# Kernel tuning notes

Measured on AMD Instinct MI355X. Metric: run time of the kernel, lower is better.

Reference implementation:

```python
import jax, jax.numpy as jnp
import numpy as np

THRESHOLD = 0.3
STRENGTH = 0.1
MIN_S = 0.0
MAX_S = 0.5
EPS_COS = 1e-8
EPS_LN = 1e-5

B, T, D = 1024, 64, 256
P = 2048
H = 512


def _layernorm(x, g, b):
    mu = x.mean(-1, keepdims=True)
    var = ((x - mu) ** 2).mean(-1, keepdims=True)
    return (x - mu) * jax.lax.rsqrt(var + EPS_LN) * g + b


def setup_inputs() -> dict:
    key = jax.random.key(0)
    ks = jax.random.split(key, 10)
    s = lambda fan_in: 1.0 / np.sqrt(fan_in)
    return {
        "current_feat": jax.random.normal(ks[0], (B, T, D), jnp.float32),
        "prototype": jax.random.normal(ks[1], (P, T, D), jnp.float32),
        "dd_w1": jax.random.normal(ks[2], (2 * D, H), jnp.float32) * s(2 * D),
        "dd_b1": jnp.zeros((H,), jnp.float32),
        "dd_g1": jnp.ones((H,), jnp.float32),
        "dd_be1": jnp.zeros((H,), jnp.float32),
        "dd_w2": jax.random.normal(ks[3], (H, H // 2), jnp.float32) * s(H),
        "dd_b2": jnp.zeros((H // 2,), jnp.float32),
        "dd_w3": jax.random.normal(ks[4], (H // 2, 1), jnp.float32) * s(H // 2),
        "dd_b3": jnp.zeros((1,), jnp.float32),
        "cal_w1": jax.random.normal(ks[5], (D, H), jnp.float32) * s(D),
        "cal_b1": jnp.zeros((H,), jnp.float32),
        "cal_g1": jnp.ones((H,), jnp.float32),
        "cal_be1": jnp.zeros((H,), jnp.float32),
        "cal_w2": jax.random.normal(ks[6], (H, H), jnp.float32) * s(H),
        "cal_b2": jnp.zeros((H,), jnp.float32),
        "cal_w3": jax.random.normal(ks[7], (H, D), jnp.float32) * s(H),
        "cal_b3": jnp.zeros((D,), jnp.float32),
    }


def reference(current_feat, prototype,
              dd_w1, dd_b1, dd_g1, dd_be1, dd_w2, dd_b2, dd_w3, dd_b3,
              cal_w1, cal_b1, cal_g1, cal_be1, cal_w2, cal_b2, cal_w3, cal_b3):
    # --- drift detection ---
    feat_flat = current_feat.mean(axis=1)          # [B, D]
    proto_centers = prototype.mean(axis=1)         # [P, D]
    fn = jnp.maximum(jnp.linalg.norm(feat_flat, axis=-1), EPS_COS)   # [B]
    pn = jnp.maximum(jnp.linalg.norm(proto_centers, axis=-1), EPS_COS)  # [P]
    sim = jnp.einsum('bd,pd->bp', feat_flat, proto_centers) / (fn[:, None] * pn[None, :])
    drift_score = 1.0 - sim                        # [B, P]
    is_drifted = drift_score.mean(axis=0) > THRESHOLD  # [P] bool

    # --- calibration (batched over all P, then masked scatter) ---
    global_mean = feat_flat.mean(axis=0)           # [D]
    concat = jnp.concatenate(
        [proto_centers, jnp.broadcast_to(global_mean, (proto_centers.shape[0], global_mean.shape[0]))], axis=-1)  # [P, 2D]
    h = jax.nn.relu(_layernorm(concat @ dd_w1 + dd_b1, dd_g1, dd_be1))
    h = jax.nn.relu(h @ dd_w2 + dd_b2)
    drift_conf = jax.nn.sigmoid(h @ dd_w3 + dd_b3)[:, 0]  # [P]

    c = jax.nn.relu(_layernorm(proto_centers @ cal_w1 + cal_b1, cal_g1, cal_be1))
    c = jax.nn.relu(c @ cal_w2 + cal_b2)
    delta = c @ cal_w3 + cal_b3                    # [P, D]

    strength = jnp.clip(STRENGTH * drift_conf, MIN_S, MAX_S)  # [P]
    new_center = proto_centers + strength[:, None] * delta    # [P, D]

    calibrated = jnp.where(is_drifted[:, None, None], new_center[:, None, :], prototype)  # [P, T, D]
    return calibrated, drift_score, is_drifted
```

## Files before the change

kernel.cpp:

```cpp
#include <hip/hip_runtime.h>
#include <hip/hip_bf16.h>
#include <math.h>

#define BB 1024
#define TT 64
#define DD 256
#define PP 2048
#define HH 512

typedef __attribute__((ext_vector_type(8))) short short8;
typedef __attribute__((ext_vector_type(4))) short short4v;
typedef __attribute__((ext_vector_type(4))) float f32x4;

__device__ __forceinline__ float4 f4add(float4 a, float4 b) {
    return make_float4(a.x + b.x, a.y + b.y, a.z + b.z, a.w + b.w);
}

__device__ __forceinline__ void nt_store4(float* p, float4 v) {
    f32x4 t = {v.x, v.y, v.z, v.w};
    __builtin_nontemporal_store(t, (f32x4*)p);
}

__device__ __forceinline__ void nt_store1(float* p, float v) {
    __builtin_nontemporal_store(v, p);
}

__device__ __forceinline__ float4 nt_load4(const float* p) {
    f32x4 t = __builtin_nontemporal_load((const f32x4*)p);
    return make_float4(t.x, t.y, t.z, t.w);
}

__device__ __forceinline__ void store_bf16x4(__hip_bfloat16* dst, float4 m) {
    union { __hip_bfloat16 h[4]; short4v s; } u;
    u.h[0] = __float2bfloat16(m.x); u.h[1] = __float2bfloat16(m.y);
    u.h[2] = __float2bfloat16(m.z); u.h[3] = __float2bfloat16(m.w);
    *(short4v*)dst = u.s;
}

__global__ void prep_k(const float* __restrict__ cf, const float* __restrict__ proto,
                       const float* __restrict__ dd_w1, const float* __restrict__ dd_w2,
                       const float* __restrict__ cal_w1, const float* __restrict__ cal_w2,
                       const float* __restrict__ cal_w3,
                       float* __restrict__ ffm, float* __restrict__ fn,
                       float* __restrict__ pn, float* __restrict__ pc,
                       float* __restrict__ colsum,
                       __hip_bfloat16* __restrict__ ffb, __hip_bfloat16* __restrict__ pcb,
                       __hip_bfloat16* __restrict__ w1cat, __hip_bfloat16* __restrict__ w2dd,
                       __hip_bfloat16* __restrict__ w2cal, __hip_bfloat16* __restrict__ w3cal) {
    int b = blockIdx.x, tid = threadIdx.x;
    if (b < 768) {
        int wv = tid >> 6, lane = tid & 63;
        int row = (b << 2) + wv;
        const float* base = (row < 1024) ? cf + (size_t)row * TT * DD
                                         : proto + (size_t)(row - 1024) * TT * DD;
        const float* p = base + (lane << 2);
        float4 acc = make_float4(0.f, 0.f, 0.f, 0.f);
        float4 v[16];
        #pragma unroll
        for (int tb = 0; tb < TT; tb += 16) {
            #pragma unroll
            for (int i = 0; i < 16; ++i)
                v[i] = nt_load4(p + (size_t)(tb + i) * DD);
            #pragma unroll
            for (int i = 0; i < 8; ++i) v[i] = f4add(v[i], v[i + 8]);
            #pragma unroll
            for (int i = 0; i < 4; ++i) v[i] = f4add(v[i], v[i + 4]);
            acc = f4add(acc, f4add(f4add(v[0], v[1]), f4add(v[2], v[3])));
        }
        float4 m = make_float4(acc.x * (1.f / TT), acc.y * (1.f / TT),
                               acc.z * (1.f / TT), acc.w * (1.f / TT));
        if (row < 1024) {
            *(float4*)(ffm + (size_t)row * DD + (lane << 2)) = m;
            store_bf16x4(ffb + (size_t)row * DD + (lane << 2), m);
        } else {
            int r = row - 1024;
            *(float4*)(pc + (size_t)r * DD + (lane << 2)) = m;
            store_bf16x4(pcb + (size_t)r * DD + (lane << 2), m);
        }
        float q = m.x * m.x + m.y * m.y + m.z * m.z + m.w * m.w;
        #pragma unroll
        for (int o = 32; o > 0; o >>= 1) q += __shfl_xor(q, o, 64);
        if (lane == 0) {
            float nv = fmaxf(sqrtf(q), 1e-8f);
            if (row < 1024) fn[row] = nv; else pn[row - 1024] = nv;
        }
    } else {
        int bb = b - 768;
        if (bb < 8) colsum[bb * 256 + tid] = 0.f;
        #pragma unroll
        for (int i2 = 0; i2 < 4; ++i2) {
            int idx = bb * 1024 + i2 * 256 + tid;
            if (idx < 262144) {
                int half = idx >> 17;
                int i = idx & 131071;
                int n = i & 511, k = i >> 9;
                const float* src = half ? cal_w1 : dd_w1;
                float x = __builtin_nontemporal_load(src + (size_t)k * 512 + n);
                w1cat[(size_t)(half * 512 + n) * 256 + k] = __float2bfloat16(x);
            } else if (idx < 393216) {
                int i = idx - 262144;
                int n = i & 255, k = i >> 8;
                float x = __builtin_nontemporal_load(dd_w2 + (size_t)k * 256 + n);
                w2dd[(size_t)n * 512 + k] = __float2bfloat16(x);
            } else if (idx < 655360) {
                int i = idx - 393216;
                int n = i & 511, k = i >> 9;
                float x = __builtin_nontemporal_load(cal_w2 + (size_t)k * 512 + n);
                w2cal[(size_t)n * 512 + k] = __float2bfloat16(x);
            } else {
                int i = idx - 655360;
                int n = i & 255, k = i >> 8;
                float x = __builtin_nontemporal_load(cal_w3 + (size_t)k * 256 + n);
                w3cal[(size_t)n * 512 + k] = __float2bfloat16(x);
            }
        }
    }
}

__global__ void sim_addvec_k(const __hip_bfloat16* __restrict__ A,
                             const __hip_bfloat16* __restrict__ Bt,
                             const float* __restrict__ fn, const float* __restrict__ pn,
                             const float* __restrict__ ffm,
                             const float* __restrict__ dd_w1, const float* __restrict__ dd_b1,
                             float* __restrict__ drift, float* __restrict__ colsum,
                             float* __restrict__ addvec) {
    if (blockIdx.x >= 512) {
        __shared__ float gmk[256];
        int tid = threadIdx.x;
        const float* f = ffm + tid;
        float a0 = 0.f, a1 = 0.f, a2 = 0.f, a3 = 0.f, a4 = 0.f, a5 = 0.f, a6 = 0.f, a7 = 0.f;
        #pragma unroll 4
        for (int b = 0; b < 1024; b += 8) {
            a0 += f[(b + 0) << 8]; a1 += f[(b + 1) << 8];
            a2 += f[(b + 2) << 8]; a3 += f[(b + 3) << 8];
            a4 += f[(b + 4) << 8]; a5 += f[(b + 5) << 8];
            a6 += f[(b + 6) << 8]; a7 += f[(b + 7) << 8];
        }
        gmk[tid] = (((a0 + a1) + (a2 + a3)) + ((a4 + a5) + (a6 + a7))) * (1.f / BB);
        __syncthreads();
        int j = (blockIdx.x - 512) * 256 + tid;
        float s = dd_b1[j];
        #pragma unroll 8
        for (int k = 0; k < 256; ++k) s = fmaf(gmk[k], dd_w1[(size_t)(256 + k) * 512 + j], s);
        addvec[j] = s;
        return;
    }
    int wid = (blockIdx.x << 2) + (threadIdx.x >> 6);
    int lane = threadIdx.x & 63;
    int mw = wid >> 6, nw = wid & 63;
    int m0 = mw << 5, n0 = nw << 5;
    int lr = lane & 15, quad = lane >> 4;
    const __hip_bfloat16* pa0 = A + (size_t)(m0 + lr) * DD + quad * 8;
    const __hip_bfloat16* pa1 = pa0 + 16 * DD;
    const __hip_bfloat16* pb0 = Bt + (size_t)(n0 + lr) * DD + quad * 8;
    const __hip_bfloat16* pb1 = pb0 + 16 * DD;
    f32x4 acc00 = {0,0,0,0}, acc01 = {0,0,0,0}, acc10 = {0,0,0,0}, acc11 = {0,0,0,0};
    #pragma unroll
    for (int k = 0; k < DD; k += 32) {
        short8 a0 = *(const short8*)(pa0 + k);
        short8 a1 = *(const short8*)(pa1 + k);
        short8 b0 = *(const short8*)(pb0 + k);
        short8 b1 = *(const short8*)(pb1 + k);
        acc00 = __builtin_amdgcn_mfma_f32_16x16x32_bf16(a0, b0, acc00, 0, 0, 0);
        acc01 = __builtin_amdgcn_mfma_f32_16x16x32_bf16(a0, b1, acc01, 0, 0, 0);
        acc10 = __builtin_amdgcn_mfma_f32_16x16x32_bf16(a1, b0, acc10, 0, 0, 0);
        acc11 = __builtin_amdgcn_mfma_f32_16x16x32_bf16(a1, b1, acc11, 0, 0, 0);
    }
    int col0 = n0 + lr, col1 = col0 + 16;
    float ip0 = 1.f / pn[col0], ip1 = 1.f / pn[col1];
    float cs0 = 0.f, cs1 = 0.f;
    #pragma unroll
    for (int r = 0; r < 4; ++r) {
        int row0 = m0 + quad * 4 + r;
        int row1 = row0 + 16;
        float if0 = 1.f / fn[row0];
        float if1 = 1.f / fn[row1];
        float d00 = 1.f - acc00[r] * if0 * ip0;
        float d01 = 1.f - acc01[r] * if0 * ip1;
        float d10 = 1.f - acc10[r] * if1 * ip0;
        float d11 = 1.f - acc11[r] * if1 * ip1;
        nt_store1(&drift[(size_t)row0 * PP + col0], d00);
        nt_store1(&drift[(size_t)row0 * PP + col1], d01);
        nt_store1(&drift[(size_t)row1 * PP + col0], d10);
        nt_store1(&drift[(size_t)row1 * PP + col1], d11);
        cs0 += d00 + d10;
        cs1 += d01 + d11;
    }
    cs0 += __shfl_xor(cs0, 16, 64); cs0 += __shfl_xor(cs0, 32, 64);
    cs1 += __shfl_xor(cs1, 16, 64); cs1 += __shfl_xor(cs1, 32, 64);
    if (quad == 0) {
        atomicAdd(&colsum[col0], cs0);
        atomicAdd(&colsum[col1], cs1);
    }
}

__global__ void gemm1ln_k(const __hip_bfloat16* __restrict__ pcb,
                          const __hip_bfloat16* __restrict__ w1cat,
                          const float* __restrict__ addvec, const float* __restrict__ cal_b1,
                          const float* __restrict__ gdd, const float* __restrict__ bedd,
                          const float* __restrict__ gcal, const float* __restrict__ becal,
                          __hip_bfloat16* __restrict__ Ydd, __hip_bfloat16* __restrict__ Ycal) {
    __shared__ float lds_s[4][32];
    __shared__ float lds_q[4][32];
    int h = blockIdx.x >> 6;
    int r0 = (blockIdx.x & 63) << 5;
    int wv = threadIdx.x >> 6;
    int lane = threadIdx.x & 63;
    int lr = lane & 15, quad = lane >> 4;
    const float* bias = h ? cal_b1 : addvec;
    const float* g    = h ? gcal : gdd;
    const float* be   = h ? becal : bedd;
    __hip_bfloat16* Y = h ? Ycal : Ydd;

    const __hip_bfloat16* pa0 = pcb + (size_t)(r0 + lr) * DD + quad * 8;
    const __hip_bfloat16* pa1 = pa0 + 16 * DD;

    f32x4 a00[4], a01[4], a10[4], a11[4];
    float bi0[4], bi1[4];
    #pragma unroll
    for (int t = 0; t < 4; ++t) {
        int n0g = h * 512 + wv * 128 + t * 32;
        const __hip_bfloat16* pb0 = w1cat + (size_t)(n0g + lr) * DD + quad * 8;
        const __hip_bfloat16* pb1 = pb0 + 16 * DD;
        f32x4 c00 = {0,0,0,0}, c01 = {0,0,0,0}, c10 = {0,0,0,0}, c11 = {0,0,0,0};
        #pragma unroll
        for (int k = 0; k < DD; k += 32) {
            short8 av0 = *(const short8*)(pa0 + k);
            short8 av1 = *(const short8*)(pa1 + k);
            short8 bv0 = *(const short8*)(pb0 + k);
            short8 bv1 = *(const short8*)(pb1 + k);
            c00 = __builtin_amdgcn_mfma_f32_16x16x32_bf16(av0, bv0, c00, 0, 0, 0);
            c01 = __builtin_amdgcn_mfma_f32_16x16x32_bf16(av0, bv1, c01, 0, 0, 0);
            c10 = __builtin_amdgcn_mfma_f32_16x16x32_bf16(av1, bv0, c10, 0, 0, 0);
            c11 = __builtin_amdgcn_mfma_f32_16x16x32_bf16(av1, bv1, c11, 0, 0, 0);
        }
        a00[t] = c00; a01[t] = c01; a10[t] = c10; a11[t] = c11;
        int cl0 = wv * 128 + t * 32 + lr;
        bi0[t] = bias[cl0];
        bi1[t] = bias[cl0 + 16];
    }

    float ps_lo[4] = {0,0,0,0}, pq_lo[4] = {0,0,0,0};
    float ps_hi[4] = {0,0,0,0}, pq_hi[4] = {0,0,0,0};
    #pragma unroll
    for (int t = 0; t < 4; ++t) {
        #pragma unroll
        for (int r = 0; r < 4; ++r) {
            float v00 = a00[t][r] + bi0[t];
            float v01 = a01[t][r] + bi1[t];
            float v10 = a10[t][r] + bi0[t];
            float v11 = a11[t][r] + bi1[t];
            a00[t][r] = v00; a01[t][r] = v01; a10[t][r] = v10; a11[t][r] = v11;
            ps_lo[r] += v00 + v01;  pq_lo[r] += v00 * v00 + v01 * v01;
            ps_hi[r] += v10 + v11;  pq_hi[r] += v10 * v10 + v11 * v11;
        }
    }
    #pragma unroll
    for (int mset = 1; mset < 16; mset <<= 1) {
        #pragma unroll
        for (int r = 0; r < 4; ++r) {
            ps_lo[r] += __shfl_xor(ps_lo[r], mset, 64);
            pq_lo[r] += __shfl_xor(pq_lo[r], mset, 64);
            ps_hi[r] += __shfl_xor(ps_hi[r], mset, 64);
            pq_hi[r] += __shfl_xor(pq_hi[r], mset, 64);
        }
    }
    if (lr < 8) {
        int rr = quad * 4 + (lr & 3) + ((lr >> 2) << 4);
        lds_s[wv][rr] = (lr >= 4) ? ps_hi[lr & 3] : ps_lo[lr & 3];
        lds_q[wv][rr] = (lr >= 4) ? pq_hi[lr & 3] : pq_lo[lr & 3];
    }
    __syncthreads();

    float mu_lo[4], rs_lo[4], mu_hi[4], rs_hi[4];
    #pragma unroll
    for (int r = 0; r < 4; ++r) {
        int rl = quad * 4 + r;
        float s = lds_s[0][rl] + lds_s[1][rl] + lds_s[2][rl] + lds_s[3][rl];
        float q = lds_q[0][rl] + lds_q[1][rl] + lds_q[2][rl] + lds_q[3][rl];
        float mu = s * (1.f / HH);
        float var = fmaxf(q * (1.f / HH) - mu * mu, 0.f);
        mu_lo[r] = mu; rs_lo[r] = rsqrtf(var + 1e-5f);
        int rh = rl + 16;
        s = lds_s[0][rh] + lds_s[1][rh] + lds_s[2][rh] + lds_s[3][rh];
        q = lds_q[0][rh] + lds_q[1][rh] + lds_q[2][rh] + lds_q[3][rh];
        mu = s * (1.f / HH);
        var = fmaxf(q * (1.f / HH) - mu * mu, 0.f);
        mu_hi[r] = mu; rs_hi[r] = rsqrtf(var + 1e-5f);
    }

    #pragma unroll
    for (int t = 0; t < 4; ++t) {
        int c0 = wv * 128 + t * 32 + lr, c1 = c0 + 16;
        float g0 = g[c0], g1 = g[c1], b0 = be[c0], b1 = be[c1];
        #pragma unroll
        for (int r = 0; r < 4; ++r) {
            int row = r0 + quad * 4 + r;
            float y00 = fmaxf((a00[t][r] - mu_lo[r]) * rs_lo[r] * g0 + b0, 0.f);
            float y01 = fmaxf((a01[t][r] - mu_lo[r]) * rs_lo[r] * g1 + b1, 0.f);
            float y10 = fmaxf((a10[t][r] - mu_hi[r]) * rs_hi[r] * g0 + b0, 0.f);
            float y11 = fmaxf((a11[t][r] - mu_hi[r]) * rs_hi[r] * g1 + b1, 0.f);
            Y[(size_t)row * HH + c0]        = __float2bfloat16(y00);
            Y[(size_t)row * HH + c1]        = __float2bfloat16(y01);
            Y[(size_t)(row + 16) * HH + c0] = __float2bfloat16(y10);
            Y[(size_t)(row + 16) * HH + c1] = __float2bfloat16(y11);
        }
    }
}

template <int K, int OUT_BF16, int RELU>
__device__ __forceinline__ void gemm_tile(const __hip_bfloat16* __restrict__ A,
                                          const __hip_bfloat16* __restrict__ Bt,
                                          const float* __restrict__ bias0,
                                          const float* __restrict__ bias1, int split,
                                          void* __restrict__ Cout, int N, int lognt,
                                          int wid, int lane) {
    int mw = wid >> lognt, nw = wid & ((1 << lognt) - 1);
    int m0 = mw << 5, n0 = nw << 5;
    int lr = lane & 15, quad = lane >> 4;
    const __hip_bfloat16* pa0 = A + (size_t)(m0 + lr) * K + quad * 8;
    const __hip_bfloat16* pa1 = pa0 + 16 * K;
    const __hip_bfloat16* pb0 = Bt + (size_t)(n0 + lr) * K + quad * 8;
    const __hip_bfloat16* pb1 = pb0 + 16 * K;
    f32x4 acc00 = {0,0,0,0}, acc01 = {0,0,0,0}, acc10 = {0,0,0,0}, acc11 = {0,0,0,0};
    #pragma unroll
    for (int k = 0; k < K; k += 32) {
        short8 a0 = *(const short8*)(pa0 + k);
        short8 a1 = *(const short8*)(pa1 + k);
        short8 b0 = *(const short8*)(pb0 + k);
        short8 b1 = *(const short8*)(pb1 + k);
        acc00 = __builtin_amdgcn_mfma_f32_16x16x32_bf16(a0, b0, acc00, 0, 0, 0);
        acc01 = __builtin_amdgcn_mfma_f32_16x16x32_bf16(a0, b1, acc01, 0, 0, 0);
        acc10 = __builtin_amdgcn_mfma_f32_16x16x32_bf16(a1, b0, acc10, 0, 0, 0);
        acc11 = __builtin_amdgcn_mfma_f32_16x16x32_bf16(a1, b1, acc11, 0, 0, 0);
    }
    int col0 = n0 + lr, col1 = col0 + 16;
    float bi0 = (col0 < split) ? bias0[col0] : bias1[col0 - split];
    float bi1 = (col1 < split) ? bias0[col1] : bias1[col1 - split];
    #pragma unroll
    for (int r = 0; r < 4; ++r) {
        int row0 = m0 + quad * 4 + r;
        int row1 = row0 + 16;
        float v00 = acc00[r] + bi0, v01 = acc01[r] + bi1;
        float v10 = acc10[r] + bi0, v11 = acc11[r] + bi1;
        if (RELU) {
            v00 = fmaxf(v00, 0.f); v01 = fmaxf(v01, 0.f);
            v10 = fmaxf(v10, 0.f); v11 = fmaxf(v11, 0.f);
        }
        if (OUT_BF16) {
            __hip_bfloat16* C = (__hip_bfloat16*)Cout;
            C[(size_t)row0 * N + col0] = __float2bfloat16(v00);
            C[(size_t)row0 * N + col1] = __float2bfloat16(v01);
            C[(size_t)row1 * N + col0] = __float2bfloat16(v10);
            C[(size_t)row1 * N + col1] = __float2bfloat16(v11);
        } else {
            float* C = (float*)Cout;
            C[(size_t)row0 * N + col0] = v00;
            C[(size_t)row0 * N + col1] = v01;
            C[(size_t)row1 * N + col0] = v10;
            C[(size_t)row1 * N + col1] = v11;
        }
    }
}

__global__ void gemm2_k(const __hip_bfloat16* __restrict__ act_dd,
                        const __hip_bfloat16* __restrict__ act_cal,
                        const __hip_bfloat16* __restrict__ w2dd,
                        const __hip_bfloat16* __restrict__ w2cal,
                        const float* __restrict__ dd_b2, const float* __restrict__ cal_b2,
                        __hip_bfloat16* __restrict__ act2b, __hip_bfloat16* __restrict__ act3b) {
    int lane = threadIdx.x & 63;
    if (blockIdx.x < 128) {
        int wid = (blockIdx.x << 2) + (threadIdx.x >> 6);
        gemm_tile<512, 1, 1>(act_dd, w2dd, dd_b2, dd_b2, 1 << 30, act2b, 256, 3, wid, lane);
    } else {
        int wid = ((blockIdx.x - 128) << 2) + (threadIdx.x >> 6);
        gemm_tile<512, 1, 1>(act_cal, w2cal, cal_b2, cal_b2, 1 << 30, act3b, 512, 4, wid, lane);
    }
}

__global__ void gemm3_conf_k(const __hip_bfloat16* __restrict__ act3b,
                             const __hip_bfloat16* __restrict__ w3cal,
                             const float* __restrict__ cal_b3,
                             const __hip_bfloat16* __restrict__ act2b,
                             const float* __restrict__ dd_w3, const float* __restrict__ dd_b3,
                             const float* __restrict__ colsum,
                             float* __restrict__ delta, float* __restrict__ strength,
                             float* __restrict__ out_is) {
    if (blockIdx.x < 128) {
        int wid = (blockIdx.x << 2) + (threadIdx.x >> 6);
        gemm_tile<512, 0, 0>(act3b, w3cal, cal_b3, cal_b3, 1 << 30, delta, 256, 3,
                             wid, threadIdx.x & 63);
        return;
    }
    int p = ((blockIdx.x - 128) << 2) + (threadIdx.x >> 6);
    int lane = threadIdx.x & 63;
    const __hip_bfloat16* row = act2b + (size_t)p * 256 + lane * 4;
    float s = 0.f;
    #pragma unroll
    for (int j = 0; j < 4; ++j)
        s += __bfloat162float(row[j]) * dd_w3[lane * 4 + j];
    #pragma unroll
    for (int o = 32; o > 0; o >>= 1) s += __shfl_down(s, o, 64);
    if (lane == 0) {
        float conf = 1.f / (1.f + expf(-(s + dd_b3[0])));
        strength[p] = fminf(fmaxf(0.1f * conf, 0.f), 0.5f);
        out_is[p] = (colsum[p] * (1.f / BB) > 0.3f) ? 1.f : 0.f;
    }
}

__global__ void finalize_k(const float* __restrict__ pc, const float* __restrict__ delta,
                           const float* __restrict__ strength, const float* __restrict__ colsum,
                           const float* __restrict__ proto, float* __restrict__ out) {
    int p = blockIdx.x;
    int d4 = (threadIdx.x & 63) << 2;
    int t0 = threadIdx.x >> 6;
    bool dr = colsum[p] * (1.f / BB) > 0.3f;
    float* o = out + (size_t)p * TT * DD;
    if (dr) {
        float s = strength[p];
        float4 pcv = *(const float4*)(pc + (size_t)p * DD + d4);
        float4 dv  = *(const float4*)(delta + (size_t)p * DD + d4);
        float4 nc = make_float4(fmaf(s, dv.x, pcv.x), fmaf(s, dv.y, pcv.y),
                                fmaf(s, dv.z, pcv.z), fmaf(s, dv.w, pcv.w));
        #pragma unroll
        for (int t = t0; t < TT; t += 4)
            nt_store4(o + t * DD + d4, nc);
    } else {
        const float* pr = proto + (size_t)p * TT * DD;
        #pragma unroll
        for (int t = t0; t < TT; t += 4)
            nt_store4(o + t * DD + d4, nt_load4(pr + t * DD + d4));
    }
}

extern "C" void kernel_launch(void* const* d_in, const int* in_sizes, int n_in,
                              void* d_out, int out_size, void* d_ws, size_t ws_size,
                              hipStream_t stream) {
    const float* cf     = (const float*)d_in[0];
    const float* proto  = (const float*)d_in[1];
    const float* dd_w1  = (const float*)d_in[2];
    const float* dd_b1  = (const float*)d_in[3];
    const float* dd_g1  = (const float*)d_in[4];
    const float* dd_be1 = (const float*)d_in[5];
    const float* dd_w2  = (const float*)d_in[6];
    const float* dd_b2  = (const float*)d_in[7];
    const float* dd_w3  = (const float*)d_in[8];
    const float* dd_b3  = (const float*)d_in[9];
    const float* cal_w1 = (const float*)d_in[10];
    const float* cal_b1 = (const float*)d_in[11];
    const float* cal_g1 = (const float*)d_in[12];
    const float* cal_be1= (const float*)d_in[13];
    const float* cal_w2 = (const float*)d_in[14];
    const float* cal_b2 = (const float*)d_in[15];
    const float* cal_w3 = (const float*)d_in[16];
    const float* cal_b3 = (const float*)d_in[17];

    float* out_cal   = (float*)d_out;
    float* out_drift = out_cal + (size_t)PP * TT * DD;
    float* out_is    = out_drift + (size_t)BB * PP;

    float* w = (float*)d_ws;
    float* colsum   = w;
    float* addvec   = w + 4096;
    float* fn       = w + 4608;
    float* pn       = w + 5632;
    float* strength = w + 7680;
    float* pc       = w + 9728;
    float* ffm      = w + 534016;
    float* delta    = w + 2631168;
    __hip_bfloat16* bb = (__hip_bfloat16*)(w + 3155456);
    __hip_bfloat16* ffb     = bb;
    __hip_bfloat16* pcb     = bb + 262144;
    __hip_bfloat16* w1cat   = bb + 786432;
    __hip_bfloat16* w2dd    = bb + 1048576;
    __hip_bfloat16* w2cal   = bb + 1179648;
    __hip_bfloat16* w3cal   = bb + 1441792;
    __hip_bfloat16* act_dd  = bb + 1572864;
    __hip_bfloat16* act_cal = bb + 2621440;
    __hip_bfloat16* act2b   = bb + 3670016;
    __hip_bfloat16* act3b   = bb + 4194304;

    prep_k<<<1536, 256, 0, stream>>>(cf, proto, dd_w1, dd_w2, cal_w1, cal_w2, cal_w3,
                                     ffm, fn, pn, pc, colsum, ffb, pcb,
                                     w1cat, w2dd, w2cal, w3cal);
    sim_addvec_k<<<514, 256, 0, stream>>>(ffb, pcb, fn, pn, ffm, dd_w1, dd_b1,
                                          out_drift, colsum, addvec);
    gemm1ln_k<<<128, 256, 0, stream>>>(pcb, w1cat, addvec, cal_b1,
                                       dd_g1, dd_be1, cal_g1, cal_be1,
                                       act_dd, act_cal);
    gemm2_k<<<384, 256, 0, stream>>>(act_dd, act_cal, w2dd, w2cal, dd_b2, cal_b2,
                                     act2b, act3b);
    gemm3_conf_k<<<640, 256, 0, stream>>>(act3b, w3cal, cal_b3, act2b, dd_w3, dd_b3,
                                          colsum, delta, strength, out_is);
    finalize_k<<<PP, 256, 0, stream>>>(pc, delta, strength, colsum, proto, out_cal);
}
```

Before: 413.2 us.

## Fuse MLP layers into one kernel keeping activations in LDS

Merges the first-layer GEMM+LayerNorm, the second-layer GEMMs, the third-layer GEMM and the confidence head into a single kernel. Each block handles 32 rows for one branch and keeps intermediate bf16 activations in padded shared memory instead of writing them to global memory. The is_drifted output moves into the finalize kernel. This removes two kernel launches and the global round trips for the activations. In exchange only 128 blocks run the whole MLP chain with serial per-block work, which may underuse the GPU compared with the earlier wider launches.

```diff
diff --git a/kernel.cpp b/kernel.cpp
--- a/kernel.cpp
+++ b/kernel.cpp
@@ -194,27 +194,35 @@
     }
 }
 
-__global__ void gemm1ln_k(const __hip_bfloat16* __restrict__ pcb,
-                          const __hip_bfloat16* __restrict__ w1cat,
-                          const float* __restrict__ addvec, const float* __restrict__ cal_b1,
-                          const float* __restrict__ gdd, const float* __restrict__ bedd,
-                          const float* __restrict__ gcal, const float* __restrict__ becal,
-                          __hip_bfloat16* __restrict__ Ydd, __hip_bfloat16* __restrict__ Ycal) {
+#define LS 520
+__global__ void __launch_bounds__(256)
+mlp_k(const __hip_bfloat16* __restrict__ pcb,
+      const __hip_bfloat16* __restrict__ w1cat,
+      const float* __restrict__ addvec, const float* __restrict__ cal_b1,
+      const float* __restrict__ gdd, const float* __restrict__ bedd,
+      const float* __restrict__ gcal, const float* __restrict__ becal,
+      const __hip_bfloat16* __restrict__ w2dd, const __hip_bfloat16* __restrict__ w2cal,
+      const float* __restrict__ dd_b2, const float* __restrict__ cal_b2,
+      const __hip_bfloat16* __restrict__ w3cal, const float* __restrict__ cal_b3,
+      const float* __restrict__ dd_w3, const float* __restrict__ dd_b3,
+      float* __restrict__ delta, float* __restrict__ strength) {
+    __shared__ __hip_bfloat16 act1[32 * LS];
+    __shared__ __hip_bfloat16 act2[32 * LS];
     __shared__ float lds_s[4][32];
     __shared__ float lds_q[4][32];
-    int h = blockIdx.x >> 6;
-    int r0 = (blockIdx.x & 63) << 5;
+
+    int h  = blockIdx.x & 1;
+    int r0 = (blockIdx.x >> 1) << 5;
     int wv = threadIdx.x >> 6;
     int lane = threadIdx.x & 63;
     int lr = lane & 15, quad = lane >> 4;
-    const float* bias = h ? cal_b1 : addvec;
-    const float* g    = h ? gcal : gdd;
-    const float* be   = h ? becal : bedd;
-    __hip_bfloat16* Y = h ? Ycal : Ydd;
+
+    const float* bias1 = h ? cal_b1 : addvec;
+    const float* g  = h ? gcal : gdd;
+    const float* be = h ? becal : bedd;
 
     const __hip_bfloat16* pa0 = pcb + (size_t)(r0 + lr) * DD + quad * 8;
     const __hip_bfloat16* pa1 = pa0 + 16 * DD;
-
     f32x4 a00[4], a01[4], a10[4], a11[4];
     float bi0[4], bi1[4];
     #pragma unroll
@@ -236,10 +244,9 @@
         }
         a00[t] = c00; a01[t] = c01; a10[t] = c10; a11[t] = c11;
         int cl0 = wv * 128 + t * 32 + lr;
-        bi0[t] = bias[cl0];
-        bi1[t] = bias[cl0 + 16];
-    }
-
+        bi0[t] = bias1[cl0];
+        bi1[t] = bias1[cl0 + 16];
+    }
     float ps_lo[4] = {0,0,0,0}, pq_lo[4] = {0,0,0,0};
     float ps_hi[4] = {0,0,0,0}, pq_hi[4] = {0,0,0,0};
     #pragma unroll
@@ -288,134 +295,112 @@
         var = fmaxf(q * (1.f / HH) - mu * mu, 0.f);
         mu_hi[r] = mu; rs_hi[r] = rsqrtf(var + 1e-5f);
     }
-
     #pragma unroll
     for (int t = 0; t < 4; ++t) {
         int c0 = wv * 128 + t * 32 + lr, c1 = c0 + 16;
         float g0 = g[c0], g1 = g[c1], b0 = be[c0], b1 = be[c1];
         #pragma unroll
         for (int r = 0; r < 4; ++r) {
-            int row = r0 + quad * 4 + r;
-            float y00 = fmaxf((a00[t][r] - mu_lo[r]) * rs_lo[r] * g0 + b0, 0.f);
-            float y01 = fmaxf((a01[t][r] - mu_lo[r]) * rs_lo[r] * g1 + b1, 0.f);
-            float y10 = fmaxf((a10[t][r] - mu_hi[r]) * rs_hi[r] * g0 + b0, 0.f);
-            float y11 = fmaxf((a11[t][r] - mu_hi[r]) * rs_hi[r] * g1 + b1, 0.f);
-            Y[(size_t)row * HH + c0]        = __float2bfloat16(y00);
-            Y[(size_t)row * HH + c1]        = __float2bfloat16(y01);
-            Y[(size_t)(row + 16) * HH + c0] = __float2bfloat16(y10);
-            Y[(size_t)(row + 16) * HH + c1] = __float2bfloat16(y11);
-        }
-    }
-}
-
-template <int K, int OUT_BF16, int RELU>
-__device__ __forceinline__ void gemm_tile(const __hip_bfloat16* __restrict__ A,
-                                          const __hip_bfloat16* __restrict__ Bt,
-                                          const float* __restrict__ bias0,
-                                          const float* __restrict__ bias1, int split,
-                                          void* __restrict__ Cout, int N, int lognt,
-                                          int wid, int lane) {
-    int mw = wid >> lognt, nw = wid & ((1 << lognt) - 1);
-    int m0 = mw << 5, n0 = nw << 5;
-    int lr = lane & 15, quad = lane >> 4;
-    const __hip_bfloat16* pa0 = A + (size_t)(m0 + lr) * K + quad * 8;
-    const __hip_bfloat16* pa1 = pa0 + 16 * K;
-    const __hip_bfloat16* pb0 = Bt + (size_t)(n0 + lr) * K + quad * 8;
-    const __hip_bfloat16* pb1 = pb0 + 16 * K;
-    f32x4 acc00 = {0,0,0,0}, acc01 = {0,0,0,0}, acc10 = {0,0,0,0}, acc11 = {0,0,0,0};
-    #pragma unroll
-    for (int k = 0; k < K; k += 32) {
-        short8 a0 = *(const short8*)(pa0 + k);
-        short8 a1 = *(const short8*)(pa1 + k);
-        short8 b0 = *(const short8*)(pb0 + k);
-        short8 b1 = *(const short8*)(pb1 + k);
-        acc00 = __builtin_amdgcn_mfma_f32_16x16x32_bf16(a0, b0, acc00, 0, 0, 0);
-        acc01 = __builtin_amdgcn_mfma_f32_16x16x32_bf16(a0, b1, acc01, 0, 0, 0);
-        acc10 = __builtin_amdgcn_mfma_f32_16x16x32_bf16(a1, b0, acc10, 0, 0, 0);
-        acc11 = __builtin_amdgcn_mfma_f32_16x16x32_bf16(a1, b1, acc11, 0, 0, 0);
-    }
-    int col0 = n0 + lr, col1 = col0 + 16;
-    float bi0 = (col0 < split) ? bias0[col0] : bias1[col0 - split];
-    float bi1 = (col1 < split) ? bias0[col1] : bias1[col1 - split];
-    #pragma unroll
-    for (int r = 0; r < 4; ++r) {
-        int row0 = m0 + quad * 4 + r;
-        int row1 = row0 + 16;
-        float v00 = acc00[r] + bi0, v01 = acc01[r] + bi1;
-        float v10 = acc10[r] + bi0, v11 = acc11[r] + bi1;
-        if (RELU) {
-            v00 = fmaxf(v00, 0.f); v01 = fmaxf(v01, 0.f);
-            v10 = fmaxf(v10, 0.f); v11 = fmaxf(v11, 0.f);
-        }
-        if (OUT_BF16) {
-            __hip_bfloat16* C = (__hip_bfloat16*)Cout;
-            C[(size_t)row0 * N + col0] = __float2bfloat16(v00);
-            C[(size_t)row0 * N + col1] = __float2bfloat16(v01);
-            C[(size_t)row1 * N + col0] = __float2bfloat16(v10);
-            C[(size_t)row1 * N + col1] = __float2bfloat16(v11);
-        } else {
-            float* C = (float*)Cout;
-            C[(size_t)row0 * N + col0] = v00;
-            C[(size_t)row0 * N + col1] = v01;
-            C[(size_t)row1 * N + col0] = v10;
-            C[(size_t)row1 * N + col1] = v11;
-        }
-    }
-}
-
-__global__ void gemm2_k(const __hip_bfloat16* __restrict__ act_dd,
-                        const __hip_bfloat16* __restrict__ act_cal,
-                        const __hip_bfloat16* __restrict__ w2dd,
-                        const __hip_bfloat16* __restrict__ w2cal,
-                        const float* __restrict__ dd_b2, const float* __restrict__ cal_b2,
-                        __hip_bfloat16* __restrict__ act2b, __hip_bfloat16* __restrict__ act3b) {
-    int lane = threadIdx.x & 63;
-    if (blockIdx.x < 128) {
-        int wid = (blockIdx.x << 2) + (threadIdx.x >> 6);
-        gemm_tile<512, 1, 1>(act_dd, w2dd, dd_b2, dd_b2, 1 << 30, act2b, 256, 3, wid, lane);
+            int rl = quad * 4 + r, rh = rl + 16;
+            act1[rl * LS + c0] = __float2bfloat16(fmaxf((a00[t][r] - mu_lo[r]) * rs_lo[r] * g0 + b0, 0.f));
+            act1[rl * LS + c1] = __float2bfloat16(fmaxf((a01[t][r] - mu_lo[r]) * rs_lo[r] * g1 + b1, 0.f));
+            act1[rh * LS + c0] = __float2bfloat16(fmaxf((a10[t][r] - mu_hi[r]) * rs_hi[r] * g0 + b0, 0.f));
+            act1[rh * LS + c1] = __float2bfloat16(fmaxf((a11[t][r] - mu_hi[r]) * rs_hi[r] * g1 + b1, 0.f));
+        }
+    }
+    __syncthreads();
+
+    {
+        const __hip_bfloat16* w2 = h ? w2cal : w2dd;
+        const float* b2 = h ? cal_b2 : dd_b2;
+        int nt2 = h ? 4 : 2;
+        #pragma unroll
+        for (int tt = 0; tt < 4; ++tt) {
+            if (tt < nt2) {
+                int n0 = wv * (nt2 << 5) + (tt << 5);
+                const __hip_bfloat16* pb0 = w2 + (size_t)(n0 + lr) * 512 + quad * 8;
+                const __hip_bfloat16* pb1 = pb0 + 16 * 512;
+                f32x4 c00 = {0,0,0,0}, c01 = {0,0,0,0}, c10 = {0,0,0,0}, c11 = {0,0,0,0};
+                #pragma unroll
+                for (int k = 0; k < 512; k += 32) {
+                    short8 av0 = *(const short8*)&act1[lr * LS + quad * 8 + k];
+                    short8 av1 = *(const short8*)&act1[(lr + 16) * LS + quad * 8 + k];
+                    short8 bv0 = *(const short8*)(pb0 + k);
+                    short8 bv1 = *(const short8*)(pb1 + k);
+                    c00 = __builtin_amdgcn_mfma_f32_16x16x32_bf16(av0, bv0, c00, 0, 0, 0);
+                    c01 = __builtin_amdgcn_mfma_f32_16x16x32_bf16(av0, bv1, c01, 0, 0, 0);
+                    c10 = __builtin_amdgcn_mfma_f32_16x16x32_bf16(av1, bv0, c10, 0, 0, 0);
+                    c11 = __builtin_amdgcn_mfma_f32_16x16x32_bf16(av1, bv1, c11, 0, 0, 0);
+                }
+                float bb0 = b2[n0 + lr], bb1 = b2[n0 + 16 + lr];
+                #pragma unroll
+                for (int r = 0; r < 4; ++r) {
+                    int rl = quad * 4 + r, rh = rl + 16;
+                    act2[rl * LS + n0 + lr]      = __float2bfloat16(fmaxf(c00[r] + bb0, 0.f));
+                    act2[rl * LS + n0 + 16 + lr] = __float2bfloat16(fmaxf(c01[r] + bb1, 0.f));
+                    act2[rh * LS + n0 + lr]      = __float2bfloat16(fmaxf(c10[r] + bb0, 0.f));
+                    act2[rh * LS + n0 + 16 + lr] = __float2bfloat16(fmaxf(c11[r] + bb1, 0.f));
+                }
+            }
+        }
+    }
+    __syncthreads();
+
+    if (h == 0) {
+        int r = threadIdx.x >> 3, e = threadIdx.x & 7;
+        float s = 0.f;
+        #pragma unroll 8
+        for (int c = 0; c < 32; ++c) {
+            int cc = e * 32 + c;
+            s += __bfloat162float(act2[r * LS + cc]) * dd_w3[cc];
+        }
+        s += __shfl_down(s, 4, 8);
+        s += __shfl_down(s, 2, 8);
+        s += __shfl_down(s, 1, 8);
+        if (e == 0) {
+            float conf = 1.f / (1.f + expf(-(s + dd_b3[0])));
+            strength[r0 + r] = fminf(fmaxf(0.1f * conf, 0.f), 0.5f);
+        }
     } else {
-        int wid = ((blockIdx.x - 128) << 2) + (threadIdx.x >> 6);
-        gemm_tile<512, 1, 1>(act_cal, w2cal, cal_b2, cal_b2, 1 << 30, act3b, 512, 4, wid, lane);
-    }
-}
-
-__global__ void gemm3_conf_k(const __hip_bfloat16* __restrict__ act3b,
-                             const __hip_bfloat16* __restrict__ w3cal,
-                             const float* __restrict__ cal_b3,
-                             const __hip_bfloat16* __restrict__ act2b,
-                             const float* __restrict__ dd_w3, const float* __restrict__ dd_b3,
-                             const float* __restrict__ colsum,
-                             float* __restrict__ delta, float* __restrict__ strength,
-                             float* __restrict__ out_is) {
-    if (blockIdx.x < 128) {
-        int wid = (blockIdx.x << 2) + (threadIdx.x >> 6);
-        gemm_tile<512, 0, 0>(act3b, w3cal, cal_b3, cal_b3, 1 << 30, delta, 256, 3,
-                             wid, threadIdx.x & 63);
-        return;
-    }
-    int p = ((blockIdx.x - 128) << 2) + (threadIdx.x >> 6);
-    int lane = threadIdx.x & 63;
-    const __hip_bfloat16* row = act2b + (size_t)p * 256 + lane * 4;
-    float s = 0.f;
-    #pragma unroll
-    for (int j = 0; j < 4; ++j)
-        s += __bfloat162float(row[j]) * dd_w3[lane * 4 + j];
-    #pragma unroll
-    for (int o = 32; o > 0; o >>= 1) s += __shfl_down(s, o, 64);
-    if (lane == 0) {
-        float conf = 1.f / (1.f + expf(-(s + dd_b3[0])));
-        strength[p] = fminf(fmaxf(0.1f * conf, 0.f), 0.5f);
-        out_is[p] = (colsum[p] * (1.f / BB) > 0.3f) ? 1.f : 0.f;
+        #pragma unroll
+        for (int tt = 0; tt < 2; ++tt) {
+            int n0 = (wv << 6) + (tt << 5);
+            const __hip_bfloat16* pb0 = w3cal + (size_t)(n0 + lr) * 512 + quad * 8;
+            const __hip_bfloat16* pb1 = pb0 + 16 * 512;
+            f32x4 c00 = {0,0,0,0}, c01 = {0,0,0,0}, c10 = {0,0,0,0}, c11 = {0,0,0,0};
+            #pragma unroll
+            for (int k = 0; k < 512; k += 32) {
+                short8 av0 = *(const short8*)&act2[lr * LS + quad * 8 + k];
+                short8 av1 = *(const short8*)&act2[(lr + 16) * LS + quad * 8 + k];
+                short8 bv0 = *(const short8*)(pb0 + k);
+                short8 bv1 = *(const short8*)(pb1 + k);
+                c00 = __builtin_amdgcn_mfma_f32_16x16x32_bf16(av0, bv0, c00, 0, 0, 0);
+                c01 = __builtin_amdgcn_mfma_f32_16x16x32_bf16(av0, bv1, c01, 0, 0, 0);
+                c10 = __builtin_amdgcn_mfma_f32_16x16x32_bf16(av1, bv0, c10, 0, 0, 0);
+                c11 = __builtin_amdgcn_mfma_f32_16x16x32_bf16(av1, bv1, c11, 0, 0, 0);
+            }
+            float bb0 = cal_b3[n0 + lr], bb1 = cal_b3[n0 + 16 + lr];
+            #pragma unroll
+            for (int r = 0; r < 4; ++r) {
+                int rl = quad * 4 + r, rh = rl + 16;
+                delta[(size_t)(r0 + rl) * 256 + n0 + lr]      = c00[r] + bb0;
+                delta[(size_t)(r0 + rl) * 256 + n0 + 16 + lr] = c01[r] + bb1;
+                delta[(size_t)(r0 + rh) * 256 + n0 + lr]      = c10[r] + bb0;
+                delta[(size_t)(r0 + rh) * 256 + n0 + 16 + lr] = c11[r] + bb1;
+            }
+        }
     }
 }
 
 __global__ void finalize_k(const float* __restrict__ pc, const float* __restrict__ delta,
                            const float* __restrict__ strength, const float* __restrict__ colsum,
-                           const float* __restrict__ proto, float* __restrict__ out) {
+                           const float* __restrict__ proto, float* __restrict__ out,
+                           float* __restrict__ out_is) {
     int p = blockIdx.x;
     int d4 = (threadIdx.x & 63) << 2;
     int t0 = threadIdx.x >> 6;
     bool dr = colsum[p] * (1.f / BB) > 0.3f;
+    if (threadIdx.x == 0) out_is[p] = dr ? 1.f : 0.f;
     float* o = out + (size_t)p * TT * DD;
     if (dr) {
         float s = strength[p];
@@ -476,22 +461,16 @@
     __hip_bfloat16* w2dd    = bb + 1048576;
     __hip_bfloat16* w2cal   = bb + 1179648;
     __hip_bfloat16* w3cal   = bb + 1441792;
-    __hip_bfloat16* act_dd  = bb + 1572864;
-    __hip_bfloat16* act_cal = bb + 2621440;
-    __hip_bfloat16* act2b   = bb + 3670016;
-    __hip_bfloat16* act3b   = bb + 4194304;
 
     prep_k<<<1536, 256, 0, stream>>>(cf, proto, dd_w1, dd_w2, cal_w1, cal_w2, cal_w3,
                                      ffm, fn, pn, pc, colsum, ffb, pcb,
                                      w1cat, w2dd, w2cal, w3cal);
     sim_addvec_k<<<514, 256, 0, stream>>>(ffb, pcb, fn, pn, ffm, dd_w1, dd_b1,
                                           out_drift, colsum, addvec);
-    gemm1ln_k<<<128, 256, 0, stream>>>(pcb, w1cat, addvec, cal_b1,
-                                       dd_g1, dd_be1, cal_g1, cal_be1,
-                                       act_dd, act_cal);
-    gemm2_k<<<384, 256, 0, stream>>>(act_dd, act_cal, w2dd, w2cal, dd_b2, cal_b2,
-                                     act2b, act3b);
-    gemm3_conf_k<<<640, 256, 0, stream>>>(act3b, w3cal, cal_b3, act2b, dd_w3, dd_b3,
-                                          colsum, delta, strength, out_is);
-    finalize_k<<<PP, 256, 0, stream>>>(pc, delta, strength, colsum, proto, out_cal);
-}
+    mlp_k<<<128, 256, 0, stream>>>(pcb, w1cat, addvec, cal_b1,
+                                   dd_g1, dd_be1, cal_g1, cal_be1,
+                                   w2dd, w2cal, dd_b2, cal_b2,
+                                   w3cal, cal_b3, dd_w3, dd_b3,
+                                   delta, strength);
+    finalize_k<<<PP, 256, 0, stream>>>(pc, delta, strength, colsum, proto, out_cal, out_is);
+}
```

After: 399.7 us. -3.3%, faster.
